# Optimization experiments

Measured on AMD Instinct MI355X. Metric: run time of the kernel, lower is better.

Reference implementation:

```python
import jax, jax.numpy as jnp
import numpy as np

NUM_EXPERTS = 16
TOP_K = 2
AUX_LOSS_COEF = 0.01


def setup_inputs() -> dict:
    key = jax.random.key(0)
    ks = jax.random.split(key, 5)
    B, S, D, I, E = 4, 2048, 1024, 2816, NUM_EXPERTS
    scale = 0.02
    return {
        "x": jax.random.normal(ks[0], (B, S, D), dtype=jnp.float32),
        "gate_w": jax.random.normal(ks[1], (D, E), dtype=jnp.float32) * scale,
        "Wg": jax.random.normal(ks[2], (E, D, I), dtype=jnp.float32) * scale,
        "Wu": jax.random.normal(ks[3], (E, D, I), dtype=jnp.float32) * scale,
        "Wd": jax.random.normal(ks[4], (E, I, D), dtype=jnp.float32) * scale,
    }


def _moe_forward(x, gate_w, Wg, Wu, Wd):
    B, S, D = x.shape
    E = gate_w.shape[1]
    # Router
    logits = x @ gate_w                      # [B,S,E]
    probs = jax.nn.softmax(logits, axis=-1)  # [B,S,E]
    topk_w, topk_idx = jax.lax.top_k(probs, TOP_K)        # [B,S,K]
    topk_w = topk_w / jnp.sum(topk_w, axis=-1, keepdims=True)
    # Per-token combine weight for each expert: [B,S,E]
    onehot = jax.nn.one_hot(topk_idx, E, dtype=x.dtype)   # [B,S,K,E]
    combine_w = jnp.einsum("bsk,bske->bse", topk_w, onehot)
    x_flat = x.reshape(-1, D)                # [T,D]
    w_flat = combine_w.reshape(-1, E)        # [T,E]
    # Accumulate weighted expert outputs (loop over fixed small E; unselected
    # tokens get zero weight, identical math to masked gather/scatter).
    out = jnp.zeros_like(x_flat)
    for e in range(E):
        h = jax.nn.silu(x_flat @ Wg[e]) * (x_flat @ Wu[e])  # [T,I]
        out = out + (h @ Wd[e]) * w_flat[:, e:e + 1]
    out = out.reshape(B, S, D)
    # Load balancing aux loss
    expert_mask = onehot.sum(axis=2)                        # [B,S,E]
    tokens_per_expert = expert_mask.mean(axis=(0, 1))       # [E]
    router_prob_per_expert = probs.mean(axis=(0, 1))        # [E]
    aux_loss = AUX_LOSS_COEF * jnp.sum(tokens_per_expert * router_prob_per_expert) * E
    return out, aux_loss


def reference(x, gate_w, Wg, Wu, Wd):
    return _moe_forward(x, gate_w, Wg, Wu, Wd)
```

## Files before the change

### kernel.cpp

```cpp
#include <hip/hip_runtime.h>
#include <stdint.h>

#define T_TOKENS 8192
#define D_DIM 1024
#define I_DIM 2816
#define E_NUM 16
#define N_SLOTS 16384

typedef float f32x4 __attribute__((ext_vector_type(4)));
typedef short s16x8 __attribute__((ext_vector_type(8)));
typedef short s16x4 __attribute__((ext_vector_type(4)));
typedef unsigned short u16;
typedef unsigned int u32;

__device__ __forceinline__ u16 f2bf(float f) {
  u32 u = __builtin_bit_cast(u32, f);
  u = (u + 0x7FFFu + ((u >> 16) & 1u)) >> 16;
  return (u16)u;
}
__device__ __forceinline__ u32 pack2(float a, float b) {
  return (u32)f2bf(a) | ((u32)f2bf(b) << 16);
}
__device__ __forceinline__ void async_load16(const void* g, void* l) {
  __builtin_amdgcn_global_load_lds(
      (const __attribute__((address_space(1))) void*)g,
      (__attribute__((address_space(3))) void*)l, 16, 0, 0);
}

__global__ void router_kernel(const float* __restrict__ x,
                              const float* __restrict__ gw,
                              int* __restrict__ e12, float* __restrict__ w12,
                              int* __restrict__ cnt, float* __restrict__ probsum) {
  __shared__ float sProb[E_NUM];
  __shared__ int sCnt[E_NUM];
  int tid = threadIdx.x;
  if (tid < E_NUM) { sProb[tid] = 0.f; sCnt[tid] = 0; }
  __syncthreads();
  int g = tid >> 4, i = tid & 15;
  int t = blockIdx.x * 16 + g;
  float acc[E_NUM];
#pragma unroll
  for (int e = 0; e < E_NUM; e++) acc[e] = 0.f;
  const f32x4* x4 = (const f32x4*)(x + (size_t)t * D_DIM);
  const f32x4* g4 = (const f32x4*)gw;
  for (int jj = 0; jj < 16; jj++) {
    f32x4 xv = x4[i + 16 * jj];
    int jb = 4 * (i + 16 * jj);
#pragma unroll
    for (int r = 0; r < 4; r++) {
      float xs = xv[r];
#pragma unroll
      for (int e4 = 0; e4 < 4; e4++) {
        f32x4 gv = g4[(jb + r) * 4 + e4];
        acc[e4 * 4 + 0] += xs * gv[0];
        acc[e4 * 4 + 1] += xs * gv[1];
        acc[e4 * 4 + 2] += xs * gv[2];
        acc[e4 * 4 + 3] += xs * gv[3];
      }
    }
  }
#pragma unroll
  for (int e = 0; e < E_NUM; e++) {
    float v = acc[e];
    v += __shfl_down(v, 8, 16);
    v += __shfl_down(v, 4, 16);
    v += __shfl_down(v, 2, 16);
    v += __shfl_down(v, 1, 16);
    acc[e] = v;
  }
  if (i == 0) {
    float mx = acc[0];
#pragma unroll
    for (int e = 1; e < E_NUM; e++) mx = fmaxf(mx, acc[e]);
    float p[E_NUM]; float s = 0.f;
#pragma unroll
    for (int e = 0; e < E_NUM; e++) { p[e] = __expf(acc[e] - mx); s += p[e]; }
    float inv = 1.f / s;
#pragma unroll
    for (int e = 0; e < E_NUM; e++) p[e] *= inv;
    int e1 = 0; float p1 = p[0];
#pragma unroll
    for (int e = 1; e < E_NUM; e++) if (p[e] > p1) { p1 = p[e]; e1 = e; }
    int e2 = (e1 == 0) ? 1 : 0; float p2 = p[e2];
#pragma unroll
    for (int e = 0; e < E_NUM; e++) if (e != e1 && p[e] > p2) { p2 = p[e]; e2 = e; }
    float wsum = p1 + p2;
    e12[2 * t] = e1; e12[2 * t + 1] = e2;
    w12[2 * t] = p1 / wsum; w12[2 * t + 1] = p2 / wsum;
#pragma unroll
    for (int e = 0; e < E_NUM; e++) atomicAdd(&sProb[e], p[e]);
    atomicAdd(&sCnt[e1], 1);
    atomicAdd(&sCnt[e2], 1);
  }
  __syncthreads();
  if (tid < E_NUM) {
    atomicAdd(&cnt[tid], sCnt[tid]);
    atomicAdd(&probsum[tid], sProb[tid]);
  }
}

__global__ void prefix_kernel(const int* __restrict__ cnt, int* __restrict__ offsets,
                              const float* __restrict__ probsum, float* __restrict__ aux_out) {
  if (threadIdx.x == 0) {
    int s = 0;
    for (int e = 0; e < E_NUM; e++) { offsets[e] = s; s += cnt[e]; }
    offsets[E_NUM] = s;
    float a = 0.f;
    for (int e = 0; e < E_NUM; e++) a += (float)cnt[e] * probsum[e];
    aux_out[0] = 0.01f * 16.f * a / (8192.f * 8192.f);
  }
}

__global__ void build_kernel(const int* __restrict__ e12, const float* __restrict__ w12,
                             const int* __restrict__ offsets, int* __restrict__ cursor,
                             int* __restrict__ tlist, float* __restrict__ wlist) {
  int t = blockIdx.x * 256 + threadIdx.x;
  if (t >= T_TOKENS) return;
#pragma unroll
  for (int k = 0; k < 2; k++) {
    int e = e12[2 * t + k];
    int pos = atomicAdd(&cursor[e], 1);
    int idx = offsets[e] + pos;
    tlist[idx] = t;
    wlist[idx] = w12[2 * t + k];
  }
}

__global__ void gather_kernel(const float* __restrict__ x, const int* __restrict__ tlist,
                              u16* __restrict__ Xe) {
  int r = blockIdx.x * 4 + (threadIdx.x >> 6);
  int lane = threadIdx.x & 63;
  int tok = tlist[r];
  const f32x4* src = (const f32x4*)(x + (size_t)tok * D_DIM);
  u32* dst = (u32*)(Xe + (size_t)r * D_DIM);
#pragma unroll
  for (int c = 0; c < 4; c++) {
    f32x4 v = src[lane + 64 * c];
    dst[(lane + 64 * c) * 2] = pack2(v[0], v[1]);
    dst[(lane + 64 * c) * 2 + 1] = pack2(v[2], v[3]);
  }
}

template <int K, int N>
__global__ __launch_bounds__(256) void transpose_kernel(const float* __restrict__ W,
                                                        u16* __restrict__ Wt) {
  __shared__ u16 tile[64][66];
  int e = blockIdx.z;
  int k0 = blockIdx.x * 64;
  int n0 = blockIdx.y * 64;
  const float* Win = W + (size_t)e * K * N;
  u16* Wout = Wt + (size_t)e * N * K;
  int t = threadIdx.x;
  int r = t >> 4;
  int c4 = (t & 15) * 4;
#pragma unroll
  for (int rep = 0; rep < 4; rep++) {
    int k = r + rep * 16;
    f32x4 v = *(const f32x4*)(Win + (size_t)(k0 + k) * N + n0 + c4);
    *(u32*)&tile[k][c4] = pack2(v[0], v[1]);
    *(u32*)&tile[k][c4 + 2] = pack2(v[2], v[3]);
  }
  __syncthreads();
#pragma unroll
  for (int rep = 0; rep < 4; rep++) {
    int n = r + rep * 16;
    int k4 = c4;
    s16x4 o;
    o[0] = tile[k4 + 0][n];
    o[1] = tile[k4 + 1][n];
    o[2] = tile[k4 + 2][n];
    o[3] = tile[k4 + 3][n];
    *(s16x4*)(Wout + (size_t)(n0 + n) * K + k0 + k4) = o;
  }
}

__global__ __launch_bounds__(512, 2) void gemm_gu_kernel(
    const u16* __restrict__ Abuf, const u16* __restrict__ Bg, const u16* __restrict__ Bu,
    u16* __restrict__ Hbuf,
    const int* __restrict__ cnt, const int* __restrict__ offsets) {
  int e = blockIdx.z;
  int Me = cnt[e];
  int m0 = blockIdx.y * 256;
  if (m0 >= Me) return;
  int n0 = blockIdx.x * 128;
  int rowBase = offsets[e];
  const u16* Bge = Bg + (size_t)e * I_DIM * D_DIM;
  const u16* Bue = Bu + (size_t)e * I_DIM * D_DIM;

  __shared__ u16 lds[65536];
  constexpr int A0 = 0, A1 = 16384;
  constexpr int Bg0 = 32768, Bg1 = 40960;
  constexpr int Bu0 = 49152, Bu1 = 57344;

  int tid = threadIdx.x;
  int lane = tid & 63;
  int wv = tid >> 6;
  int wm = wv >> 1;
  int wn = wv & 1;
  int lrow = lane & 15, lq = lane >> 4;
  int swz = lrow & 7;

  f32x4 accg[4][4], accu[4][4];
#pragma unroll
  for (int a = 0; a < 4; a++)
#pragma unroll
    for (int b = 0; b < 4; b++) { accg[a][b] = (f32x4)0.f; accu[a][b] = (f32x4)0.f; }

  auto STAGE = [&](int kt, int b) {
    int k0 = kt << 6;
#pragma unroll
    for (int r = 0; r < 4; r++) {
      int c = tid + 512 * r;
      int row = c >> 3, slot = c & 7;
      int gr = m0 + row; gr = (gr < Me) ? gr : (Me - 1);
      const u16* src = Abuf + (size_t)(rowBase + gr) * D_DIM + k0 + ((slot ^ (row & 7)) << 3);
      async_load16(src, (void*)&lds[(b ? A1 : A0) + (wv * 64 + 512 * r) * 8]);
    }
#pragma unroll
    for (int r = 0; r < 2; r++) {
      int c = tid + 512 * r;
      int row = c >> 3, slot = c & 7;
      int col = k0 + ((slot ^ (row & 7)) << 3);
      int ldso = (wv * 64 + 512 * r) * 8;
      async_load16(Bge + (size_t)(n0 + row) * D_DIM + col, (void*)&lds[(b ? Bg1 : Bg0) + ldso]);
      async_load16(Bue + (size_t)(n0 + row) * D_DIM + col, (void*)&lds[(b ? Bu1 : Bu0) + ldso]);
    }
  };

  STAGE(0, 0);
  STAGE(1, 1);

  for (int kt = 0; kt < 16; kt++) {
    int cur = kt & 1;
    if (kt < 15) asm volatile("s_waitcnt vmcnt(8)");
    else         asm volatile("s_waitcnt vmcnt(0)");
    __builtin_amdgcn_s_barrier();
    __builtin_amdgcn_sched_barrier(0);

    const u16* As = lds + (cur ? A1 : A0);
    const u16* Bgs = lds + (cur ? Bg1 : Bg0);
    const u16* Bus = lds + (cur ? Bu1 : Bu0);

#pragma unroll
    for (int kh = 0; kh < 2; kh++) {
      s16x8 af[4], bb[4];
      int so = ((kh * 4 + lq) ^ swz) << 3;
#pragma unroll
      for (int fm = 0; fm < 4; fm++) {
        int row = wm * 64 + fm * 16 + lrow;
        af[fm] = *(const s16x8*)&As[row * 64 + so];
      }
#pragma unroll
      for (int fn = 0; fn < 4; fn++) {
        int row = wn * 64 + fn * 16 + lrow;
        bb[fn] = *(const s16x8*)&Bgs[row * 64 + so];
      }
      __builtin_amdgcn_s_barrier();
      __builtin_amdgcn_s_setprio(1);
#pragma unroll
      for (int fm = 0; fm < 4; fm++)
#pragma unroll
        for (int fn = 0; fn < 4; fn++)
          accg[fm][fn] = __builtin_amdgcn_mfma_f32_16x16x32_bf16(af[fm], bb[fn], accg[fm][fn], 0, 0, 0);
      __builtin_amdgcn_s_setprio(0);
      __builtin_amdgcn_s_barrier();
#pragma unroll
      for (int fn = 0; fn < 4; fn++) {
        int row = wn * 64 + fn * 16 + lrow;
        bb[fn] = *(const s16x8*)&Bus[row * 64 + so];
      }
      __builtin_amdgcn_s_barrier();
      __builtin_amdgcn_s_setprio(1);
#pragma unroll
      for (int fm = 0; fm < 4; fm++)
#pragma unroll
        for (int fn = 0; fn < 4; fn++)
          accu[fm][fn] = __builtin_amdgcn_mfma_f32_16x16x32_bf16(af[fm], bb[fn], accu[fm][fn], 0, 0, 0);
      __builtin_amdgcn_s_setprio(0);
      __builtin_amdgcn_s_barrier();
    }

    __builtin_amdgcn_sched_barrier(0);
    if (kt + 2 < 16) STAGE(kt + 2, cur);
  }

#pragma unroll
  for (int fm = 0; fm < 4; fm++) {
#pragma unroll
    for (int i = 0; i < 4; i++) {
      int m = m0 + wm * 64 + fm * 16 + lq * 4 + i;
      if (m >= Me) continue;
      size_t arow = (size_t)(rowBase + m);
#pragma unroll
      for (int fn = 0; fn < 4; fn++) {
        int col = n0 + wn * 64 + fn * 16 + lrow;
        float g = accg[fm][fn][i];
        float u = accu[fm][fn][i];
        float h = (g / (1.f + __expf(-g))) * u;
        Hbuf[arow * I_DIM + col] = f2bf(h);
      }
    }
  }
}

__global__ __launch_bounds__(256) void gemm_down_kernel(
    const u16* __restrict__ Abuf, const u16* __restrict__ Bd, float* __restrict__ out,
    const int* __restrict__ cnt, const int* __restrict__ offsets,
    const int* __restrict__ tlist, const float* __restrict__ wlist) {
  int e = blockIdx.z;
  int Me = cnt[e];
  int m0 = blockIdx.y * 128;
  if (m0 >= Me) return;
  int n0 = blockIdx.x * 128;
  int rowBase = offsets[e];
  const u16* Bde = Bd + (size_t)e * D_DIM * I_DIM;

  __shared__ u16 Ash[128 * 32];
  __shared__ u16 Bsh[128 * 32];

  int tid = threadIdx.x;
  int lane = tid & 63;
  int wv = tid >> 6;
  int mq = wv & 1, nq = wv >> 1;
  int lrow = lane & 15, lq = lane >> 4;

  f32x4 acc[4][4];
#pragma unroll
  for (int a = 0; a < 4; a++)
#pragma unroll
    for (int b = 0; b < 4; b++) acc[a][b] = (f32x4)0.f;

  for (int k0 = 0; k0 < I_DIM; k0 += 32) {
#pragma unroll
    for (int rep = 0; rep < 2; rep++) {
      int idx = tid + 256 * rep;
      int row = idx >> 2, q = idx & 3;
      int ldso = (wv * 64 + 256 * rep) * 8;
      int gr = m0 + row;
      gr = (gr < Me) ? gr : (Me - 1);
      async_load16(Abuf + (size_t)(rowBase + gr) * I_DIM + k0 + q * 8, &Ash[ldso]);
      async_load16(Bde + (size_t)(n0 + row) * I_DIM + k0 + q * 8, &Bsh[ldso]);
    }
    __syncthreads();
    s16x8 af[4], bfr[4];
#pragma unroll
    for (int fm = 0; fm < 4; fm++)
      af[fm] = *(const s16x8*)&Ash[(mq * 64 + fm * 16 + lrow) * 32 + lq * 8];
#pragma unroll
    for (int fn = 0; fn < 4; fn++)
      bfr[fn] = *(const s16x8*)&Bsh[(nq * 64 + fn * 16 + lrow) * 32 + lq * 8];
#pragma unroll
    for (int fm = 0; fm < 4; fm++)
#pragma unroll
      for (int fn = 0; fn < 4; fn++)
        acc[fm][fn] = __builtin_amdgcn_mfma_f32_16x16x32_bf16(af[fm], bfr[fn], acc[fm][fn], 0, 0, 0);
    __syncthreads();
  }
#pragma unroll
  for (int fm = 0; fm < 4; fm++) {
#pragma unroll
    for (int i = 0; i < 4; i++) {
      int m = m0 + mq * 64 + fm * 16 + lq * 4 + i;
      if (m >= Me) continue;
      size_t arow = (size_t)(rowBase + m);
      int tok = tlist[arow];
      float w = wlist[arow];
#pragma unroll
      for (int fn = 0; fn < 4; fn++) {
        int col = n0 + nq * 64 + fn * 16 + lrow;
        atomicAdd(&out[(size_t)tok * D_DIM + col], acc[fm][fn][i] * w);
      }
    }
  }
}

extern "C" void kernel_launch(void* const* d_in, const int* in_sizes, int n_in,
                              void* d_out, int out_size, void* d_ws, size_t ws_size,
                              hipStream_t stream) {
  const float* x  = (const float*)d_in[0];
  const float* gw = (const float*)d_in[1];
  const float* Wg = (const float*)d_in[2];
  const float* Wu = (const float*)d_in[3];
  const float* Wd = (const float*)d_in[4];
  float* outf = (float*)d_out;
  char* ws = (char*)d_ws;
  int*   cnt     = (int*)(ws + 0);
  int*   cursor  = (int*)(ws + 64);
  float* probsum = (float*)(ws + 128);
  int*   offsets = (int*)(ws + 192);
  int*   e12     = (int*)(ws + 512);
  float* w12     = (float*)(ws + 66048);
  int*   tlist   = (int*)(ws + 131584);
  float* wlist   = (float*)(ws + 197120);
  u16*   Xe      = (u16*)(ws + (1 << 20));
  u16*   H       = (u16*)(ws + 34603008);
  u16*   WtA     = (u16*)(ws + 134217728);
  u16*   WtB     = (u16*)(ws + 234881024);

  hipMemsetAsync(d_out, 0, (size_t)(T_TOKENS * D_DIM + 1) * sizeof(float), stream);
  hipMemsetAsync(d_ws, 0, 512, stream);

  router_kernel<<<512, 256, 0, stream>>>(x, gw, e12, w12, cnt, probsum);
  prefix_kernel<<<1, 64, 0, stream>>>(cnt, offsets, probsum, outf + (size_t)(T_TOKENS * D_DIM));
  build_kernel<<<32, 256, 0, stream>>>(e12, w12, offsets, cursor, tlist, wlist);
  gather_kernel<<<4096, 256, 0, stream>>>(x, tlist, Xe);

  transpose_kernel<D_DIM, I_DIM><<<dim3(16, 44, E_NUM), 256, 0, stream>>>(Wg, WtA);
  transpose_kernel<D_DIM, I_DIM><<<dim3(16, 44, E_NUM), 256, 0, stream>>>(Wu, WtB);

  gemm_gu_kernel<<<dim3(22, 32, E_NUM), 512, 0, stream>>>(Xe, WtA, WtB, H, cnt, offsets);

  transpose_kernel<I_DIM, D_DIM><<<dim3(44, 16, E_NUM), 256, 0, stream>>>(Wd, WtA);

  gemm_down_kernel<<<dim3(8, 64, E_NUM), 256, 0, stream>>>(H, WtA, outf, cnt, offsets, tlist, wlist);
}
```

Baseline: 1.135 ms.

## Replace atomic scatter in down GEMM with slot buffer and combine kernel

```diff
diff --git a/kernel.cpp b/kernel.cpp
--- a/kernel.cpp
+++ b/kernel.cpp
@@ -113,7 +113,8 @@
 
 __global__ void build_kernel(const int* __restrict__ e12, const float* __restrict__ w12,
                              const int* __restrict__ offsets, int* __restrict__ cursor,
-                             int* __restrict__ tlist, float* __restrict__ wlist) {
+                             int* __restrict__ tlist, float* __restrict__ wlist,
+                             int* __restrict__ slot2) {
   int t = blockIdx.x * 256 + threadIdx.x;
   if (t >= T_TOKENS) return;
 #pragma unroll
@@ -123,6 +124,7 @@
     int idx = offsets[e] + pos;
     tlist[idx] = t;
     wlist[idx] = w12[2 * t + k];
+    slot2[2 * t + k] = idx;
   }
 }
 
@@ -304,9 +306,9 @@
 }
 
 __global__ __launch_bounds__(256) void gemm_down_kernel(
-    const u16* __restrict__ Abuf, const u16* __restrict__ Bd, float* __restrict__ out,
+    const u16* __restrict__ Abuf, const u16* __restrict__ Bd, float* __restrict__ Y,
     const int* __restrict__ cnt, const int* __restrict__ offsets,
-    const int* __restrict__ tlist, const float* __restrict__ wlist) {
+    const float* __restrict__ wlist) {
   int e = blockIdx.z;
   int Me = cnt[e];
   int m0 = blockIdx.y * 128;
@@ -363,15 +365,27 @@
       int m = m0 + mq * 64 + fm * 16 + lq * 4 + i;
       if (m >= Me) continue;
       size_t arow = (size_t)(rowBase + m);
-      int tok = tlist[arow];
       float w = wlist[arow];
 #pragma unroll
       for (int fn = 0; fn < 4; fn++) {
         int col = n0 + nq * 64 + fn * 16 + lrow;
-        atomicAdd(&out[(size_t)tok * D_DIM + col], acc[fm][fn][i] * w);
-      }
-    }
-  }
+        Y[arow * D_DIM + col] = acc[fm][fn][i] * w;
+      }
+    }
+  }
+}
+
+__global__ __launch_bounds__(256) void combine_kernel(
+    const float* __restrict__ Y, const int* __restrict__ slot2,
+    float* __restrict__ out) {
+  int t = blockIdx.x;
+  int tid = threadIdx.x;
+  int s1 = slot2[2 * t];
+  int s2 = slot2[2 * t + 1];
+  const f32x4* y1 = (const f32x4*)(Y + (size_t)s1 * D_DIM);
+  const f32x4* y2 = (const f32x4*)(Y + (size_t)s2 * D_DIM);
+  f32x4* o = (f32x4*)(out + (size_t)t * D_DIM);
+  o[tid] = y1[tid] + y2[tid];
 }
 
 extern "C" void kernel_launch(void* const* d_in, const int* in_sizes, int n_in,
@@ -392,17 +406,18 @@
   float* w12     = (float*)(ws + 66048);
   int*   tlist   = (int*)(ws + 131584);
   float* wlist   = (float*)(ws + 197120);
+  int*   slot2   = (int*)(ws + 262656);
   u16*   Xe      = (u16*)(ws + (1 << 20));
   u16*   H       = (u16*)(ws + 34603008);
   u16*   WtA     = (u16*)(ws + 134217728);
   u16*   WtB     = (u16*)(ws + 234881024);
-
-  hipMemsetAsync(d_out, 0, (size_t)(T_TOKENS * D_DIM + 1) * sizeof(float), stream);
+  float* Y       = (float*)(ws + 234881024);
+
   hipMemsetAsync(d_ws, 0, 512, stream);
 
   router_kernel<<<512, 256, 0, stream>>>(x, gw, e12, w12, cnt, probsum);
   prefix_kernel<<<1, 64, 0, stream>>>(cnt, offsets, probsum, outf + (size_t)(T_TOKENS * D_DIM));
-  build_kernel<<<32, 256, 0, stream>>>(e12, w12, offsets, cursor, tlist, wlist);
+  build_kernel<<<32, 256, 0, stream>>>(e12, w12, offsets, cursor, tlist, wlist, slot2);
   gather_kernel<<<4096, 256, 0, stream>>>(x, tlist, Xe);
 
   transpose_kernel<D_DIM, I_DIM><<<dim3(16, 44, E_NUM), 256, 0, stream>>>(Wg, WtA);
@@ -412,5 +427,7 @@
 
   transpose_kernel<I_DIM, D_DIM><<<dim3(44, 16, E_NUM), 256, 0, stream>>>(Wd, WtA);
 
-  gemm_down_kernel<<<dim3(8, 64, E_NUM), 256, 0, stream>>>(H, WtA, outf, cnt, offsets, tlist, wlist);
-}
+  gemm_down_kernel<<<dim3(8, 64, E_NUM), 256, 0, stream>>>(H, WtA, Y, cnt, offsets, wlist);
+
+  combine_kernel<<<T_TOKENS, 256, 0, stream>>>(Y, slot2, outf);
+}
```

New measurement: 1.127 ms. About the same (-0.8%).
